# Optimization experiments

Hardware: AMD Instinct MI355X
Metric: run time of the kernel (lower is better)

## Reference

```python
import jax, jax.numpy as jnp
import numpy as np

N = 1_000_000
IN_DIM = 128
OUT_DIM = 128
NUM_SEGMENTS = 16384
EPS = 1e-5


def setup_inputs() -> dict:
    key = jax.random.key(0)
    k1, k2, k3, k4, k5 = jax.random.split(key, 5)
    x = jax.random.normal(k1, (N, IN_DIM), dtype=jnp.float32)
    batch = jnp.sort(jax.random.randint(k2, (N,), 0, NUM_SEGMENTS, dtype=jnp.int64))
    # Linear params (Kaiming-ish uniform like torch default)
    bound = 1.0 / np.sqrt(IN_DIM)
    W = jax.random.uniform(k3, (OUT_DIM, IN_DIM), dtype=jnp.float32, minval=-bound, maxval=bound)
    b = jax.random.uniform(k4, (OUT_DIM,), dtype=jnp.float32, minval=-bound, maxval=bound)
    # LayerNorm affine params
    ln_w = jnp.ones((OUT_DIM,), dtype=jnp.float32)
    ln_b = jnp.zeros((OUT_DIM,), dtype=jnp.float32)
    return {"x": x, "batch": batch, "W": W, "b": b, "ln_w": ln_w, "ln_b": ln_b}


def reference(x, batch, W, b, ln_w, ln_b):
    # Linear: [N, IN] @ [IN, OUT] + b
    h = jnp.einsum('ni,oi->no', x, W) + b
    # LayerNorm over last dim
    mean = jnp.mean(h, axis=-1, keepdims=True)
    var = jnp.mean(jnp.square(h - mean), axis=-1, keepdims=True)
    h = (h - mean) * jax.lax.rsqrt(var + EPS) * ln_w + ln_b
    # scatter mean over segment ids (torch_scatter: sum / clamp(count, 1))
    seg_sum = jax.ops.segment_sum(h, batch, num_segments=NUM_SEGMENTS)
    count = jax.ops.segment_sum(jnp.ones((h.shape[0],), dtype=h.dtype), batch,
                                num_segments=NUM_SEGMENTS)
    out = seg_sum / jnp.maximum(count, 1.0)[:, None]
    return out
```

## Files before the change

kernel.cpp:

```cpp
#include <hip/hip_runtime.h>
#include <hip/hip_bf16.h>

#define NROWS 1000000
#define DIM 128
#define NSEG 16384
#define TILE_M 32
#define NT (NROWS / TILE_M)
#define XH_STRIDE 136
#define HB_STRIDE (TILE_M + 1)
#define GRID1 2048
#define EPSV 1e-5f

typedef __bf16 bf16x8 __attribute__((ext_vector_type(8)));
typedef __bf16 bf16x4 __attribute__((ext_vector_type(4)));
typedef float  f32x4  __attribute__((ext_vector_type(4)));

__global__ __launch_bounds__(256, 2)
void fused_lin_ln_scatter(const float* __restrict__ x,
                          const int*   __restrict__ batch,
                          const float* __restrict__ W,
                          const float* __restrict__ bias,
                          const float* __restrict__ lnw,
                          const float* __restrict__ lnb,
                          float* __restrict__ out) {
    __shared__ __align__(16) __bf16 xh[TILE_M * XH_STRIDE];
    __shared__ float  hbuf[DIM * HB_STRIDE];
    __shared__ float2 stat2[2][TILE_M];
    __shared__ int    ibuf[TILE_M];

    const int t    = threadIdx.x;
    const int wave = t >> 6;
    const int lane = t & 63;
    const int q    = lane >> 4;
    const int l15  = lane & 15;
    const int rg   = wave >> 1;
    const int fh   = wave & 1;
    const int fbase = fh * 64;

    bf16x8 whf[4][4], wlf[4][4];
    #pragma unroll
    for (int nt = 0; nt < 4; ++nt) {
        const int f = fbase + nt * 16 + l15;
        #pragma unroll
        for (int ks = 0; ks < 4; ++ks) {
            const int k0 = ks * 32 + q * 8;
            const float4* wp = (const float4*)(W + f * DIM + k0);
            float4 a = wp[0], c = wp[1];
            float wv[8] = {a.x, a.y, a.z, a.w, c.x, c.y, c.z, c.w};
            bf16x8 hi, lo;
            #pragma unroll
            for (int j = 0; j < 8; ++j) {
                __bf16 h = (__bf16)wv[j];
                hi[j] = h;
                lo[j] = (__bf16)(wv[j] - (float)h);
            }
            whf[nt][ks] = hi;
            wlf[nt][ks] = lo;
        }
    }
    float bb[4], lwv[4], lbv[4];
    #pragma unroll
    for (int nt = 0; nt < 4; ++nt) {
        const int f = fbase + nt * 16 + l15;
        bb[nt] = bias[f];
        lwv[nt] = lnw[f];
        lbv[nt] = lnb[f];
    }

    int it = blockIdx.x;
    float4 xr[4];
    int ibv = 0;
    {
        const float4* xp = (const float4*)(x + (size_t)it * TILE_M * DIM);
        #pragma unroll
        for (int j = 0; j < 4; ++j) xr[j] = xp[t + 256 * j];
        if (t < TILE_M) ibv = batch[it * TILE_M + t];
    }

    for (; it < NT; it += GRID1) {
        #pragma unroll
        for (int j = 0; j < 4; ++j) {
            const int idx = t + 256 * j;
            const int row = idx >> 5;
            const int c4  = (idx & 31) * 4;
            float4 v = xr[j];
            bf16x4 pk = {(__bf16)v.x, (__bf16)v.y, (__bf16)v.z, (__bf16)v.w};
            *(bf16x4*)&xh[row * XH_STRIDE + c4] = pk;
        }
        if (t < TILE_M) ibuf[t] = ibv;
        __syncthreads();

        const int itn = it + GRID1;
        if (itn < NT) {
            const float4* xp = (const float4*)(x + (size_t)itn * TILE_M * DIM);
            #pragma unroll
            for (int j = 0; j < 4; ++j) xr[j] = xp[t + 256 * j];
            if (t < TILE_M) ibv = batch[itn * TILE_M + t];
        }

        f32x4 acc[4];
        #pragma unroll
        for (int nt = 0; nt < 4; ++nt) acc[nt] = (f32x4){0.f, 0.f, 0.f, 0.f};
        const int row_l = rg * 16 + l15;
        #pragma unroll
        for (int ks = 0; ks < 4; ++ks) {
            bf16x8 af = *(const bf16x8*)&xh[row_l * XH_STRIDE + ks * 32 + q * 8];
            #pragma unroll
            for (int nt = 0; nt < 4; ++nt) {
                acc[nt] = __builtin_amdgcn_mfma_f32_16x16x32_bf16(af, whf[nt][ks], acc[nt], 0, 0, 0);
                acc[nt] = __builtin_amdgcn_mfma_f32_16x16x32_bf16(af, wlf[nt][ks], acc[nt], 0, 0, 0);
            }
        }

        float s[4], sq[4];
        #pragma unroll
        for (int r = 0; r < 4; ++r) {
            float a0 = acc[0][r] + bb[0], a1 = acc[1][r] + bb[1];
            float a2 = acc[2][r] + bb[2], a3 = acc[3][r] + bb[3];
            s[r]  = a0 + a1 + a2 + a3;
            sq[r] = a0 * a0 + a1 * a1 + a2 * a2 + a3 * a3;
            #pragma unroll
            for (int m = 1; m < 16; m <<= 1) {
                s[r]  += __shfl_xor(s[r],  m, 64);
                sq[r] += __shfl_xor(sq[r], m, 64);
            }
        }
        if (l15 == 0) {
            #pragma unroll
            for (int r = 0; r < 4; ++r)
                stat2[fh][rg * 16 + q * 4 + r] = make_float2(s[r], sq[r]);
        }
        __syncthreads();

        #pragma unroll
        for (int r = 0; r < 4; ++r) {
            const int row = rg * 16 + q * 4 + r;
            float2 u0 = stat2[0][row], u1 = stat2[1][row];
            float mean = (u0.x + u1.x) * (1.0f / 128.0f);
            float var  = (u0.y + u1.y) * (1.0f / 128.0f) - mean * mean;
            float rs   = rsqrtf(var + EPSV);
            #pragma unroll
            for (int nt = 0; nt < 4; ++nt) {
                const int f = fbase + nt * 16 + l15;
                float hv = acc[nt][r] + bb[nt];
                hbuf[f * HB_STRIDE + row] = (hv - mean) * rs * lwv[nt] + lbv[nt];
            }
        }
        __syncthreads();

        {
            const int f  = t & 127;
            const int r0 = (t >> 7) * 16;
            int seg = ibuf[r0];
            float a = 0.f;
            #pragma unroll
            for (int r = 0; r < 16; ++r) {
                const int sg = ibuf[r0 + r];
                const float v = hbuf[f * HB_STRIDE + r0 + r];
                if (sg != seg) {
                    atomicAdd(out + (size_t)seg * DIM + f, a);
                    a = 0.f;
                    seg = sg;
                }
                a += v;
            }
            atomicAdd(out + (size_t)seg * DIM + f, a);
        }
        __syncthreads();
    }
}

__device__ __forceinline__ int lower_bound_seg(const int* __restrict__ batch, int v) {
    int lo = 0, hi = NROWS;
    while (lo < hi) {
        int m = (lo + hi) >> 1;
        if (batch[m] < v) lo = m + 1; else hi = m;
    }
    return lo;
}

__global__ __launch_bounds__(256)
void finalize_divide(float* __restrict__ out, const int* __restrict__ batch) {
    __shared__ float cnt[2];
    const int t = threadIdx.x;
    if (t < 2) {
        const int s = blockIdx.x * 2 + t;
        int c = lower_bound_seg(batch, s + 1) - lower_bound_seg(batch, s);
        cnt[t] = (float)max(c, 1);
    }
    __syncthreads();
    const size_t i = (size_t)blockIdx.x * 256 + t;
    out[i] = out[i] / cnt[t >> 7];
}

extern "C" void kernel_launch(void* const* d_in, const int* in_sizes, int n_in,
                              void* d_out, int out_size, void* d_ws, size_t ws_size,
                              hipStream_t stream) {
    const float* x     = (const float*)d_in[0];
    const int*   batch = (const int*)d_in[1];
    const float* W     = (const float*)d_in[2];
    const float* bias  = (const float*)d_in[3];
    const float* lnw   = (const float*)d_in[4];
    const float* lnb   = (const float*)d_in[5];
    float* out = (float*)d_out;

    hipMemsetAsync(out, 0, (size_t)out_size * sizeof(float), stream);
    fused_lin_ln_scatter<<<GRID1, 256, 0, stream>>>(x, batch, W, bias, lnw, lnb, out);
    finalize_divide<<<(NSEG * DIM) / 256, 256, 0, stream>>>(out, batch);
}
```

Before: 761.3 us.

## Drop bf16 split-weight MFMA, reduce segments in registers, raise occupancy

Removes the lo-part bf16 weight correction so each tile issues half the MFMAs, and seeds the accumulators with the bias. The shared hbuf transpose and its extra barrier are gone: normalized values stay in registers, are reduced across lanes with shuffles when a 16-row group lies in one segment, and otherwise go out as per-lane run-length atomics. Lower register and LDS use allows 3 blocks per CU with a smaller persistent grid. The trade is lower GEMM precision (plain bf16 weights) and possibly more atomics in mixed-segment groups.

```diff
diff --git a/kernel.cpp b/kernel.cpp
--- a/kernel.cpp
+++ b/kernel.cpp
@@ -7,15 +7,14 @@
 #define TILE_M 32
 #define NT (NROWS / TILE_M)
 #define XH_STRIDE 136
-#define HB_STRIDE (TILE_M + 1)
-#define GRID1 2048
+#define GRID1 768
 #define EPSV 1e-5f
 
 typedef __bf16 bf16x8 __attribute__((ext_vector_type(8)));
 typedef __bf16 bf16x4 __attribute__((ext_vector_type(4)));
 typedef float  f32x4  __attribute__((ext_vector_type(4)));
 
-__global__ __launch_bounds__(256, 2)
+__global__ __launch_bounds__(256, 3)
 void fused_lin_ln_scatter(const float* __restrict__ x,
                           const int*   __restrict__ batch,
                           const float* __restrict__ W,
@@ -24,7 +23,6 @@
                           const float* __restrict__ lnb,
                           float* __restrict__ out) {
     __shared__ __align__(16) __bf16 xh[TILE_M * XH_STRIDE];
-    __shared__ float  hbuf[DIM * HB_STRIDE];
     __shared__ float2 stat2[2][TILE_M];
     __shared__ int    ibuf[TILE_M];
 
@@ -37,7 +35,7 @@
     const int fh   = wave & 1;
     const int fbase = fh * 64;
 
-    bf16x8 whf[4][4], wlf[4][4];
+    bf16x8 whf[4][4];
     #pragma unroll
     for (int nt = 0; nt < 4; ++nt) {
         const int f = fbase + nt * 16 + l15;
@@ -47,22 +45,17 @@
             const float4* wp = (const float4*)(W + f * DIM + k0);
             float4 a = wp[0], c = wp[1];
             float wv[8] = {a.x, a.y, a.z, a.w, c.x, c.y, c.z, c.w};
-            bf16x8 hi, lo;
-            #pragma unroll
-            for (int j = 0; j < 8; ++j) {
-                __bf16 h = (__bf16)wv[j];
-                hi[j] = h;
-                lo[j] = (__bf16)(wv[j] - (float)h);
-            }
+            bf16x8 hi;
+            #pragma unroll
+            for (int j = 0; j < 8; ++j) hi[j] = (__bf16)wv[j];
             whf[nt][ks] = hi;
-            wlf[nt][ks] = lo;
         }
     }
     float bb[4], lwv[4], lbv[4];
     #pragma unroll
     for (int nt = 0; nt < 4; ++nt) {
         const int f = fbase + nt * 16 + l15;
-        bb[nt] = bias[f];
+        bb[nt]  = bias[f];
         lwv[nt] = lnw[f];
         lbv[nt] = lnb[f];
     }
@@ -90,6 +83,12 @@
         if (t < TILE_M) ibuf[t] = ibv;
         __syncthreads();
 
+        const int s_first = ibuf[rg * 16];
+        const int s_last  = ibuf[rg * 16 + 15];
+        int sgr[4];
+        #pragma unroll
+        for (int r = 0; r < 4; ++r) sgr[r] = ibuf[rg * 16 + q * 4 + r];
+
         const int itn = it + GRID1;
         if (itn < NT) {
             const float4* xp = (const float4*)(x + (size_t)itn * TILE_M * DIM);
@@ -100,38 +99,33 @@
 
         f32x4 acc[4];
         #pragma unroll
-        for (int nt = 0; nt < 4; ++nt) acc[nt] = (f32x4){0.f, 0.f, 0.f, 0.f};
+        for (int nt = 0; nt < 4; ++nt)
+            acc[nt] = (f32x4){bb[nt], bb[nt], bb[nt], bb[nt]};
         const int row_l = rg * 16 + l15;
         #pragma unroll
         for (int ks = 0; ks < 4; ++ks) {
             bf16x8 af = *(const bf16x8*)&xh[row_l * XH_STRIDE + ks * 32 + q * 8];
             #pragma unroll
-            for (int nt = 0; nt < 4; ++nt) {
+            for (int nt = 0; nt < 4; ++nt)
                 acc[nt] = __builtin_amdgcn_mfma_f32_16x16x32_bf16(af, whf[nt][ks], acc[nt], 0, 0, 0);
-                acc[nt] = __builtin_amdgcn_mfma_f32_16x16x32_bf16(af, wlf[nt][ks], acc[nt], 0, 0, 0);
+        }
+
+        #pragma unroll
+        for (int r = 0; r < 4; ++r) {
+            float s  = acc[0][r] + acc[1][r] + acc[2][r] + acc[3][r];
+            float sq = acc[0][r] * acc[0][r] + acc[1][r] * acc[1][r]
+                     + acc[2][r] * acc[2][r] + acc[3][r] * acc[3][r];
+            #pragma unroll
+            for (int m = 1; m < 16; m <<= 1) {
+                s  += __shfl_xor(s,  m, 64);
+                sq += __shfl_xor(sq, m, 64);
             }
-        }
-
-        float s[4], sq[4];
-        #pragma unroll
-        for (int r = 0; r < 4; ++r) {
-            float a0 = acc[0][r] + bb[0], a1 = acc[1][r] + bb[1];
-            float a2 = acc[2][r] + bb[2], a3 = acc[3][r] + bb[3];
-            s[r]  = a0 + a1 + a2 + a3;
-            sq[r] = a0 * a0 + a1 * a1 + a2 * a2 + a3 * a3;
-            #pragma unroll
-            for (int m = 1; m < 16; m <<= 1) {
-                s[r]  += __shfl_xor(s[r],  m, 64);
-                sq[r] += __shfl_xor(sq[r], m, 64);
-            }
-        }
-        if (l15 == 0) {
-            #pragma unroll
-            for (int r = 0; r < 4; ++r)
-                stat2[fh][rg * 16 + q * 4 + r] = make_float2(s[r], sq[r]);
+            if (l15 == 0)
+                stat2[fh][rg * 16 + q * 4 + r] = make_float2(s, sq);
         }
         __syncthreads();
 
+        float nv[4][4];
         #pragma unroll
         for (int r = 0; r < 4; ++r) {
             const int row = rg * 16 + q * 4 + r;
@@ -140,33 +134,35 @@
             float var  = (u0.y + u1.y) * (1.0f / 128.0f) - mean * mean;
             float rs   = rsqrtf(var + EPSV);
             #pragma unroll
+            for (int nt = 0; nt < 4; ++nt)
+                nv[nt][r] = (acc[nt][r] - mean) * rs * lwv[nt] + lbv[nt];
+        }
+
+        if (s_first == s_last) {
+            #pragma unroll
+            for (int nt = 0; nt < 4; ++nt) {
+                float v = nv[nt][0] + nv[nt][1] + nv[nt][2] + nv[nt][3];
+                v += __shfl_xor(v, 16, 64);
+                v += __shfl_xor(v, 32, 64);
+                if (q == 0)
+                    atomicAdd(out + (size_t)s_first * DIM + fbase + nt * 16 + l15, v);
+            }
+        } else {
+            #pragma unroll
             for (int nt = 0; nt < 4; ++nt) {
                 const int f = fbase + nt * 16 + l15;
-                float hv = acc[nt][r] + bb[nt];
-                hbuf[f * HB_STRIDE + row] = (hv - mean) * rs * lwv[nt] + lbv[nt];
+                float a = nv[nt][0];
+                #pragma unroll
+                for (int r = 1; r < 4; ++r) {
+                    if (sgr[r] != sgr[r - 1]) {
+                        atomicAdd(out + (size_t)sgr[r - 1] * DIM + f, a);
+                        a = 0.f;
+                    }
+                    a += nv[nt][r];
+                }
+                atomicAdd(out + (size_t)sgr[3] * DIM + f, a);
             }
         }
-        __syncthreads();
-
-        {
-            const int f  = t & 127;
-            const int r0 = (t >> 7) * 16;
-            int seg = ibuf[r0];
-            float a = 0.f;
-            #pragma unroll
-            for (int r = 0; r < 16; ++r) {
-                const int sg = ibuf[r0 + r];
-                const float v = hbuf[f * HB_STRIDE + r0 + r];
-                if (sg != seg) {
-                    atomicAdd(out + (size_t)seg * DIM + f, a);
-                    a = 0.f;
-                    seg = sg;
-                }
-                a += v;
-            }
-            atomicAdd(out + (size_t)seg * DIM + f, a);
-        }
-        __syncthreads();
     }
 }
 
```

Measured after the change: 742.9 us. 2.4% less time.
